# Kernel tuning notes

Hardware: AMD Instinct MI355X
Metric: run time of the kernel (lower is better)

The kernel has to match this reference:

```python
import jax, jax.numpy as jnp
import numpy as np

HEADSIZE = 64  # Attention 'channels' arg: per-head dim used by split_heads and the scale


def setup_inputs() -> dict:
    key = jax.random.key(0)
    # [B, C, T, H, W]; C must equal channels*heads = 512 (channel_split constraint)
    x = jax.random.normal(key, (4, 512, 8, 14, 14), dtype=jnp.float32)
    return {"x": x}


def _attention(x):
    # qkv = SplitIdentity(3): repeat along channels then split back -> q = k = v = x
    B, C, T, H, W = x.shape
    N = T * H * W
    # Tokenizer.tokenize with token_dim=None: permute(0, T, H, W, C) -> [B, N, C]
    tok = jnp.transpose(x, (0, 2, 3, 4, 1)).reshape(B, N, C)
    # split_heads: reshape(B, N, headsize, heads).permute(0, 3, 1, 2) -> [B, h, N, d]
    q = tok.reshape(B, N, HEADSIZE, -1).transpose(0, 3, 1, 2)
    # qkv_aggregate: double scaling (q*s) @ (k^T * s), softmax, @ v ; s = d**-0.5
    scale = HEADSIZE ** -0.5
    scores = jnp.einsum('bhnd,bhmd->bhnm', q * scale, q * scale)  # [B,h,N,N]
    attn = jax.nn.softmax(scores, axis=-1)
    out = jnp.einsum('bhnm,bhmd->bhnd', attn, q)
    # merge_heads: permute(0, 2, 3, 1).reshape(B, N, d*h) — inverse of split_heads
    merged = out.transpose(0, 2, 3, 1).reshape(B, N, C)
    # untokenize: [B, T, H, W, C] -> [B, C, T, H, W]; proj = identity, dropouts p=0
    return merged.reshape(B, T, H, W, C).transpose(0, 4, 1, 2, 3)


def reference(x):
    return _attention(x)
```

## Files before the change

kernel.cpp:

```cpp
#include <hip/hip_runtime.h>

typedef _Float16 f16x8 __attribute__((ext_vector_type(8)));
typedef _Float16 f16x4 __attribute__((ext_vector_type(4)));
typedef float    f32x4 __attribute__((ext_vector_type(4)));
typedef unsigned int u32x4 __attribute__((ext_vector_type(4)));

constexpr int NTOK   = 1568;
constexpr int NHEADS = 8;
constexpr int NCH    = 512;
constexpr int NC32   = 52;
constexpr float SK   = 0.15014030f;
constexpr size_t IMG_BH = (size_t)NC32 * 4096;

__global__ __launch_bounds__(256)
void prep_kernel(const float* __restrict__ x, char* __restrict__ Kimg, char* __restrict__ Vimg)
{
    const int bh = blockIdx.x, c32 = blockIdx.y;
    const int b = bh >> 3, h = bh & 7;
    const int t = threadIdx.x;
    const int f = t >> 6, l = t & 63, l15 = l & 15, grp = l >> 4;

    char* Kg = Kimg + (size_t)bh * IMG_BH + (size_t)(c32 * 4 + f) * 1024 + l * 16;
    char* Vg = Vimg + (size_t)bh * IMG_BH + (size_t)(c32 * 4 + f) * 1024 + l * 16;

    const int n0 = c32 * 32;
    if (n0 >= NTOK) {
        f16x8 z;
#pragma unroll
        for (int j = 0; j < 8; ++j) z[j] = (_Float16)0.f;
        *(f16x8*)Kg = z; *(f16x8*)Vg = z;
        return;
    }

    __shared__ _Float16 kbuf[32][72];
    __shared__ _Float16 vbuf[64][40];

    const int tok = t & 31, dhi = t >> 5;
#pragma unroll
    for (int p = 0; p < 8; ++p) {
        const int d = 8 * p + dhi;
        const float v = x[((size_t)b * NCH + d * NHEADS + h) * NTOK + n0 + tok];
        kbuf[tok][d] = (_Float16)(v * SK);
        vbuf[d][tok] = (_Float16)v;
    }
    __syncthreads();

    *(f16x8*)Kg = *(const f16x8*)&kbuf[(f >> 1) * 16 + l15][(f & 1) * 32 + grp * 8];
    f16x4 va = *(const f16x4*)&vbuf[f * 16 + l15][4 * grp];
    f16x4 vb = *(const f16x4*)&vbuf[f * 16 + l15][16 + 4 * grp];
    f16x8 vv;
#pragma unroll
    for (int j = 0; j < 4; ++j) { vv[j] = va[j]; vv[4 + j] = vb[j]; }
    *(f16x8*)Vg = vv;
}

static __device__ __forceinline__ f16x8 make_bp(f32x4 sA, f32x4 sB)
{
    u32x4 w;
    w[0] = __builtin_bit_cast(unsigned int,
        __builtin_amdgcn_cvt_pkrtz(__builtin_amdgcn_exp2f(sA[0]), __builtin_amdgcn_exp2f(sA[1])));
    w[1] = __builtin_bit_cast(unsigned int,
        __builtin_amdgcn_cvt_pkrtz(__builtin_amdgcn_exp2f(sA[2]), __builtin_amdgcn_exp2f(sA[3])));
    w[2] = __builtin_bit_cast(unsigned int,
        __builtin_amdgcn_cvt_pkrtz(__builtin_amdgcn_exp2f(sB[0]), __builtin_amdgcn_exp2f(sB[1])));
    w[3] = __builtin_bit_cast(unsigned int,
        __builtin_amdgcn_cvt_pkrtz(__builtin_amdgcn_exp2f(sB[2]), __builtin_amdgcn_exp2f(sB[3])));
    return __builtin_bit_cast(f16x8, w);
}

static __device__ __forceinline__ void chunk_compute(
    const f16x8& k0, const f16x8& k1, const f16x8& k2, const f16x8& k3,
    const f16x8& v0, const f16x8& v1, const f16x8& v2, const f16x8& v3,
    const f16x8 (&aq)[2], const f16x8& ones,
    f32x4 (&oacc)[4], f32x4& lacc)
{
    const f32x4 z4 = {0.f, 0.f, 0.f, 0.f};
    f32x4 sA = __builtin_amdgcn_mfma_f32_16x16x32_f16(k0, aq[0], z4, 0, 0, 0);
    sA = __builtin_amdgcn_mfma_f32_16x16x32_f16(k1, aq[1], sA, 0, 0, 0);
    f32x4 sB = __builtin_amdgcn_mfma_f32_16x16x32_f16(k2, aq[0], z4, 0, 0, 0);
    sB = __builtin_amdgcn_mfma_f32_16x16x32_f16(k3, aq[1], sB, 0, 0, 0);
    const f16x8 bp = make_bp(sA, sB);
    lacc    = __builtin_amdgcn_mfma_f32_16x16x32_f16(ones, bp, lacc, 0, 0, 0);
    oacc[0] = __builtin_amdgcn_mfma_f32_16x16x32_f16(v0, bp, oacc[0], 0, 0, 0);
    oacc[1] = __builtin_amdgcn_mfma_f32_16x16x32_f16(v1, bp, oacc[1], 0, 0, 0);
    oacc[2] = __builtin_amdgcn_mfma_f32_16x16x32_f16(v2, bp, oacc[2], 0, 0, 0);
    oacc[3] = __builtin_amdgcn_mfma_f32_16x16x32_f16(v3, bp, oacc[3], 0, 0, 0);
}

__global__ __launch_bounds__(256, 3)
void attn_fwd(const char* __restrict__ Kimg, const char* __restrict__ Vimg,
              float* __restrict__ out)
{
    const int orig = blockIdx.x;
    const int wgid = (orig & 7) * 100 + (orig >> 3);
    const int qt = wgid % 25, bh = wgid / 25;
    const int b = bh >> 3, head = bh & 7;
    const int t = threadIdx.x, wave = t >> 6, lane = t & 63;
    const int l15 = lane & 15, grp = lane >> 4;

    __shared__ __align__(16) char kls[2][4096];
    __shared__ __align__(16) char vls[2][4096];

    const char* Kb = Kimg + (size_t)bh * IMG_BH;
    const char* Vb = Vimg + (size_t)bh * IMG_BH;

    const int s16 = qt * 4 + wave;
    f16x8 aq[2];
#pragma unroll
    for (int ks = 0; ks < 2; ++ks)
        aq[ks] = *(const f16x8*)(Kb + (size_t)(s16 * 2 + ks) * 1024 + lane * 16);

    f16x8 ones;
#pragma unroll
    for (int j = 0; j < 8; ++j) ones[j] = (_Float16)1.f;

    f32x4 oacc[4];
    f32x4 lacc = {0.f, 0.f, 0.f, 0.f};
#pragma unroll
    for (int db = 0; db < 4; ++db) oacc[db] = f32x4{0.f, 0.f, 0.f, 0.f};

    const int soff = t * 16;

    {
        f16x8 sk = *(const f16x8*)(Kb + soff);
        f16x8 sv = *(const f16x8*)(Vb + soff);
        *(f16x8*)&kls[0][soff] = sk;
        *(f16x8*)&vls[0][soff] = sv;
    }
    __syncthreads();

    for (int c = 0; c < 49; ++c) {
        const int cur = c & 1, nxt = cur ^ 1;

        f16x8 sk = *(const f16x8*)(Kb + (size_t)(c + 1) * 4096 + soff);
        f16x8 sv = *(const f16x8*)(Vb + (size_t)(c + 1) * 4096 + soff);

        f16x8 k0 = *(const f16x8*)&kls[cur][lane * 16];
        f16x8 k1 = *(const f16x8*)&kls[cur][1024 + lane * 16];
        f16x8 k2 = *(const f16x8*)&kls[cur][2048 + lane * 16];
        f16x8 k3 = *(const f16x8*)&kls[cur][3072 + lane * 16];
        f16x8 v0 = *(const f16x8*)&vls[cur][lane * 16];
        f16x8 v1 = *(const f16x8*)&vls[cur][1024 + lane * 16];
        f16x8 v2 = *(const f16x8*)&vls[cur][2048 + lane * 16];
        f16x8 v3 = *(const f16x8*)&vls[cur][3072 + lane * 16];
        chunk_compute(k0, k1, k2, k3, v0, v1, v2, v3, aq, ones, oacc, lacc);

        *(f16x8*)&kls[nxt][soff] = sk;
        *(f16x8*)&vls[nxt][soff] = sv;
        __syncthreads();
    }

    if (s16 < 98) {
        const int qrow = s16 * 16 + l15;
        const float inv = 1.0f / lacc[0];
#pragma unroll
        for (int db = 0; db < 4; ++db)
#pragma unroll
            for (int q = 0; q < 4; ++q) {
                const int d = db * 16 + 4 * grp + q;
                out[((size_t)b * NCH + (size_t)d * NHEADS + head) * NTOK + qrow] = oacc[db][q] * inv;
            }
    }
}

extern "C" void kernel_launch(void* const* d_in, const int* in_sizes, int n_in,
                              void* d_out, int out_size, void* d_ws, size_t ws_size,
                              hipStream_t stream)
{
    const float* x = (const float*)d_in[0];
    float* out     = (float*)d_out;

    char* Kimg = (char*)d_ws;
    char* Vimg = (char*)d_ws + 32 * IMG_BH;

    dim3 pgrid(32, NC32);
    prep_kernel<<<pgrid, 256, 0, stream>>>(x, Kimg, Vimg);

    attn_fwd<<<800, 256, 0, stream>>>(Kimg, Vimg, out);
}
```

Before: 46.44 us.

## Stream K/V chunks into a six-deep LDS ring via direct global-to-LDS loads

Measured after the change: 52.17 us. 1.12x slower.

```diff
diff --git a/kernel.cpp b/kernel.cpp
--- a/kernel.cpp
+++ b/kernel.cpp
@@ -87,6 +87,18 @@
     oacc[3] = __builtin_amdgcn_mfma_f32_16x16x32_f16(v3, bp, oacc[3], 0, 0, 0);
 }
 
+static __device__ __forceinline__ void stage_chunk(const char* Kb, const char* Vb,
+                                                   char* ringbase, int c, int slot,
+                                                   int wave, int lane)
+{
+    const char* gk = Kb + (size_t)c * 4096 + wave * 1024 + lane * 16;
+    const char* gv = Vb + (size_t)c * 4096 + wave * 1024 + lane * 16;
+    char* lk = ringbase + slot * 8192 + wave * 1024;
+    char* lv = ringbase + slot * 8192 + 4096 + wave * 1024;
+    __builtin_amdgcn_global_load_lds(gk, lk, 16, 0, 0);
+    __builtin_amdgcn_global_load_lds(gv, lv, 16, 0, 0);
+}
+
 __global__ __launch_bounds__(256, 3)
 void attn_fwd(const char* __restrict__ Kimg, const char* __restrict__ Vimg,
               float* __restrict__ out)
@@ -98,17 +110,18 @@
     const int t = threadIdx.x, wave = t >> 6, lane = t & 63;
     const int l15 = lane & 15, grp = lane >> 4;
 
-    __shared__ __align__(16) char kls[2][4096];
-    __shared__ __align__(16) char vls[2][4096];
+    __shared__ __align__(16) char ring[6][8192];
+    char* ringbase = &ring[0][0];
 
     const char* Kb = Kimg + (size_t)bh * IMG_BH;
     const char* Vb = Vimg + (size_t)bh * IMG_BH;
 
     const int s16 = qt * 4 + wave;
     f16x8 aq[2];
-#pragma unroll
-    for (int ks = 0; ks < 2; ++ks)
-        aq[ks] = *(const f16x8*)(Kb + (size_t)(s16 * 2 + ks) * 1024 + lane * 16);
+    aq[0] = *(const f16x8*)(Kb + (size_t)(s16 * 2 + 0) * 1024 + lane * 16);
+    aq[1] = *(const f16x8*)(Kb + (size_t)(s16 * 2 + 1) * 1024 + lane * 16);
+    asm volatile("s_waitcnt vmcnt(0)" ::: "memory");
+    __builtin_amdgcn_sched_barrier(0);
 
     f16x8 ones;
 #pragma unroll
@@ -119,35 +132,37 @@
 #pragma unroll
     for (int db = 0; db < 4; ++db) oacc[db] = f32x4{0.f, 0.f, 0.f, 0.f};
 
-    const int soff = t * 16;
+#pragma unroll
+    for (int c = 0; c < 6; ++c)
+        stage_chunk(Kb, Vb, ringbase, c, c, wave, lane);
 
-    {
-        f16x8 sk = *(const f16x8*)(Kb + soff);
-        f16x8 sv = *(const f16x8*)(Vb + soff);
-        *(f16x8*)&kls[0][soff] = sk;
-        *(f16x8*)&vls[0][soff] = sv;
-    }
-    __syncthreads();
+    int slot = 0;
+    for (int c = 0; c < 49; ++c) {
+        asm volatile("s_waitcnt vmcnt(10)" ::: "memory");
+        __builtin_amdgcn_sched_barrier(0);
+        __builtin_amdgcn_s_barrier();
+        __builtin_amdgcn_sched_barrier(0);
 
-    for (int c = 0; c < 49; ++c) {
-        const int cur = c & 1, nxt = cur ^ 1;
-
-        f16x8 sk = *(const f16x8*)(Kb + (size_t)(c + 1) * 4096 + soff);
-        f16x8 sv = *(const f16x8*)(Vb + (size_t)(c + 1) * 4096 + soff);
-
-        f16x8 k0 = *(const f16x8*)&kls[cur][lane * 16];
-        f16x8 k1 = *(const f16x8*)&kls[cur][1024 + lane * 16];
-        f16x8 k2 = *(const f16x8*)&kls[cur][2048 + lane * 16];
-        f16x8 k3 = *(const f16x8*)&kls[cur][3072 + lane * 16];
-        f16x8 v0 = *(const f16x8*)&vls[cur][lane * 16];
-        f16x8 v1 = *(const f16x8*)&vls[cur][1024 + lane * 16];
-        f16x8 v2 = *(const f16x8*)&vls[cur][2048 + lane * 16];
-        f16x8 v3 = *(const f16x8*)&vls[cur][3072 + lane * 16];
+        const char* basep = ringbase + slot * 8192;
+        f16x8 k0 = *(const f16x8*)(basep + lane * 16);
+        f16x8 k1 = *(const f16x8*)(basep + 1024 + lane * 16);
+        f16x8 k2 = *(const f16x8*)(basep + 2048 + lane * 16);
+        f16x8 k3 = *(const f16x8*)(basep + 3072 + lane * 16);
+        f16x8 v0 = *(const f16x8*)(basep + 4096 + lane * 16);
+        f16x8 v1 = *(const f16x8*)(basep + 5120 + lane * 16);
+        f16x8 v2 = *(const f16x8*)(basep + 6144 + lane * 16);
+        f16x8 v3 = *(const f16x8*)(basep + 7168 + lane * 16);
         chunk_compute(k0, k1, k2, k3, v0, v1, v2, v3, aq, ones, oacc, lacc);
 
-        *(f16x8*)&kls[nxt][soff] = sk;
-        *(f16x8*)&vls[nxt][soff] = sv;
-        __syncthreads();
+        asm volatile("s_waitcnt lgkmcnt(0)" ::: "memory");
+        __builtin_amdgcn_sched_barrier(0);
+        __builtin_amdgcn_s_barrier();
+        __builtin_amdgcn_sched_barrier(0);
+
+        const int sc = (c + 6 < 52) ? (c + 6) : 51;
+        stage_chunk(Kb, Vb, ringbase, sc, slot, wave, lane);
+
+        slot = (slot == 5) ? 0 : slot + 1;
     }
 
     if (s16 < 98) {
```

## Split key range across wave pairs with 512-thread blocks and LDS combine

Applied to the files above, without the earlier changes.

New measurement: 48.30 us. 1.04x slower.

```diff
diff --git a/kernel.cpp b/kernel.cpp
--- a/kernel.cpp
+++ b/kernel.cpp
@@ -69,17 +69,24 @@
 }
 
 static __device__ __forceinline__ void chunk_compute(
-    const f16x8& k0, const f16x8& k1, const f16x8& k2, const f16x8& k3,
-    const f16x8& v0, const f16x8& v1, const f16x8& v2, const f16x8& v3,
+    const char* kb, const char* vb, int lane,
     const f16x8 (&aq)[2], const f16x8& ones,
     f32x4 (&oacc)[4], f32x4& lacc)
 {
     const f32x4 z4 = {0.f, 0.f, 0.f, 0.f};
+    f16x8 k0 = *(const f16x8*)(kb + lane * 16);
+    f16x8 k1 = *(const f16x8*)(kb + 1024 + lane * 16);
+    f16x8 k2 = *(const f16x8*)(kb + 2048 + lane * 16);
+    f16x8 k3 = *(const f16x8*)(kb + 3072 + lane * 16);
     f32x4 sA = __builtin_amdgcn_mfma_f32_16x16x32_f16(k0, aq[0], z4, 0, 0, 0);
     sA = __builtin_amdgcn_mfma_f32_16x16x32_f16(k1, aq[1], sA, 0, 0, 0);
     f32x4 sB = __builtin_amdgcn_mfma_f32_16x16x32_f16(k2, aq[0], z4, 0, 0, 0);
     sB = __builtin_amdgcn_mfma_f32_16x16x32_f16(k3, aq[1], sB, 0, 0, 0);
     const f16x8 bp = make_bp(sA, sB);
+    f16x8 v0 = *(const f16x8*)(vb + lane * 16);
+    f16x8 v1 = *(const f16x8*)(vb + 1024 + lane * 16);
+    f16x8 v2 = *(const f16x8*)(vb + 2048 + lane * 16);
+    f16x8 v3 = *(const f16x8*)(vb + 3072 + lane * 16);
     lacc    = __builtin_amdgcn_mfma_f32_16x16x32_f16(ones, bp, lacc, 0, 0, 0);
     oacc[0] = __builtin_amdgcn_mfma_f32_16x16x32_f16(v0, bp, oacc[0], 0, 0, 0);
     oacc[1] = __builtin_amdgcn_mfma_f32_16x16x32_f16(v1, bp, oacc[1], 0, 0, 0);
@@ -87,7 +94,7 @@
     oacc[3] = __builtin_amdgcn_mfma_f32_16x16x32_f16(v3, bp, oacc[3], 0, 0, 0);
 }
 
-__global__ __launch_bounds__(256, 3)
+__global__ __launch_bounds__(512, 4)
 void attn_fwd(const char* __restrict__ Kimg, const char* __restrict__ Vimg,
               float* __restrict__ out)
 {
@@ -96,19 +103,20 @@
     const int qt = wgid % 25, bh = wgid / 25;
     const int b = bh >> 3, head = bh & 7;
     const int t = threadIdx.x, wave = t >> 6, lane = t & 63;
+    const int qs = wave >> 1, kh = wave & 1;
     const int l15 = lane & 15, grp = lane >> 4;
 
-    __shared__ __align__(16) char kls[2][4096];
-    __shared__ __align__(16) char vls[2][4096];
+    __shared__ __align__(16) char smem[36864];
+    char* ring0 = smem;
+    char* ring1 = smem + 16384;
 
     const char* Kb = Kimg + (size_t)bh * IMG_BH;
     const char* Vb = Vimg + (size_t)bh * IMG_BH;
 
-    const int s16 = qt * 4 + wave;
+    const int s16 = qt * 4 + qs;
     f16x8 aq[2];
-#pragma unroll
-    for (int ks = 0; ks < 2; ++ks)
-        aq[ks] = *(const f16x8*)(Kb + (size_t)(s16 * 2 + ks) * 1024 + lane * 16);
+    aq[0] = *(const f16x8*)(Kb + (size_t)(s16 * 2 + 0) * 1024 + lane * 16);
+    aq[1] = *(const f16x8*)(Kb + (size_t)(s16 * 2 + 1) * 1024 + lane * 16);
 
     f16x8 ones;
 #pragma unroll
@@ -124,35 +132,45 @@
     {
         f16x8 sk = *(const f16x8*)(Kb + soff);
         f16x8 sv = *(const f16x8*)(Vb + soff);
-        *(f16x8*)&kls[0][soff] = sk;
-        *(f16x8*)&vls[0][soff] = sv;
+        *(f16x8*)(ring0 + soff) = sk;
+        *(f16x8*)(ring0 + 8192 + soff) = sv;
     }
     __syncthreads();
 
-    for (int c = 0; c < 49; ++c) {
-        const int cur = c & 1, nxt = cur ^ 1;
+    for (int c = 0; c < 25; ++c) {
+        char* cur = (c & 1) ? ring1 : ring0;
+        char* nxt = (c & 1) ? ring0 : ring1;
 
-        f16x8 sk = *(const f16x8*)(Kb + (size_t)(c + 1) * 4096 + soff);
-        f16x8 sv = *(const f16x8*)(Vb + (size_t)(c + 1) * 4096 + soff);
+        f16x8 sk = *(const f16x8*)(Kb + (size_t)(c + 1) * 8192 + soff);
+        f16x8 sv = *(const f16x8*)(Vb + (size_t)(c + 1) * 8192 + soff);
 
-        f16x8 k0 = *(const f16x8*)&kls[cur][lane * 16];
-        f16x8 k1 = *(const f16x8*)&kls[cur][1024 + lane * 16];
-        f16x8 k2 = *(const f16x8*)&kls[cur][2048 + lane * 16];
-        f16x8 k3 = *(const f16x8*)&kls[cur][3072 + lane * 16];
-        f16x8 v0 = *(const f16x8*)&vls[cur][lane * 16];
-        f16x8 v1 = *(const f16x8*)&vls[cur][1024 + lane * 16];
-        f16x8 v2 = *(const f16x8*)&vls[cur][2048 + lane * 16];
-        f16x8 v3 = *(const f16x8*)&vls[cur][3072 + lane * 16];
-        chunk_compute(k0, k1, k2, k3, v0, v1, v2, v3, aq, ones, oacc, lacc);
+        chunk_compute(cur + kh * 4096, cur + 8192 + kh * 4096, lane, aq, ones, oacc, lacc);
 
-        *(f16x8*)&kls[nxt][soff] = sk;
-        *(f16x8*)&vls[nxt][soff] = sv;
+        *(f16x8*)(nxt + soff) = sk;
+        *(f16x8*)(nxt + 8192 + soff) = sv;
         __syncthreads();
     }
 
-    if (s16 < 98) {
+    float* comb = (float*)smem;
+    if (kh == 1) {
+        float* p = comb + (size_t)(qs * 64 + lane) * 17;
+#pragma unroll
+        for (int db = 0; db < 4; ++db)
+#pragma unroll
+            for (int q = 0; q < 4; ++q) p[db * 4 + q] = oacc[db][q];
+        p[16] = lacc[0];
+    }
+    __syncthreads();
+
+    if (kh == 0 && s16 < 98) {
+        const float* p = comb + (size_t)(qs * 64 + lane) * 17;
+#pragma unroll
+        for (int db = 0; db < 4; ++db)
+#pragma unroll
+            for (int q = 0; q < 4; ++q) oacc[db][q] += p[db * 4 + q];
+        const float lsum = lacc[0] + p[16] - 32.0f;
         const int qrow = s16 * 16 + l15;
-        const float inv = 1.0f / lacc[0];
+        const float inv = 1.0f / lsum;
 #pragma unroll
         for (int db = 0; db < 4; ++db)
 #pragma unroll
@@ -176,5 +194,5 @@
     dim3 pgrid(32, NC32);
     prep_kernel<<<pgrid, 256, 0, stream>>>(x, Kimg, Vimg);
 
-    attn_fwd<<<800, 256, 0, stream>>>(Kimg, Vimg, out);
+    attn_fwd<<<800, 512, 0, stream>>>(Kimg, Vimg, out);
 }
```
